# Kernel optimization log

Hardware: AMD Instinct MI355X
Metric: run time of the kernel (lower is better)

Reference implementation:

```python
import jax, jax.numpy as jnp
import numpy as np

TEMPERATURE = 0.07
BASE_TEMPERATURE = 0.07


def setup_inputs() -> dict:
    key = jax.random.key(0)
    k1, k2 = jax.random.split(key)
    features = jax.random.normal(k1, (4096, 2, 128), dtype=jnp.float32)
    labels = jax.random.randint(k2, (4096,), 0, 100, dtype=jnp.int64)
    return {"features": features, "labels": labels}


def reference(features, labels):
    # features: [B, n_views, D], labels: [B]
    B, n_views, D = features.shape
    N = B * n_views

    # label equality mask [B, B]
    lab = labels.reshape(-1, 1)
    mask = (lab == lab.T).astype(jnp.float32)

    # flatten views (C-order, same as torch .view) and L2-normalize
    feat = features.reshape(N, D)
    feat = feat / jnp.clip(jnp.linalg.norm(feat, axis=1, keepdims=True), 1e-12)

    # similarity logits [N, N]
    logits = jnp.matmul(feat, feat.T) / TEMPERATURE
    logits_max = jax.lax.stop_gradient(jnp.max(logits, axis=1, keepdims=True))
    logits = logits - logits_max

    # tile mask to [N, N] (torch .repeat ordering) and remove self-contrast
    mask = jnp.tile(mask, (n_views, n_views))
    logits_mask = 1.0 - jnp.eye(N, dtype=jnp.float32)
    mask = mask * logits_mask

    exp_logits = jnp.exp(logits) * logits_mask
    log_prob = logits - jnp.log(jnp.sum(exp_logits, axis=1, keepdims=True) + 1e-12)

    mask_pos_pairs = jnp.clip(jnp.sum(mask, axis=1), 1.0)
    mean_log_prob_pos = jnp.sum(mask * log_prob, axis=1) / mask_pos_pairs

    loss = -(TEMPERATURE / BASE_TEMPERATURE) * mean_log_prob_pos
    return jnp.mean(loss.reshape(n_views, B))
```

## Files before the change

kernel.cpp:

```cpp
#include <hip/hip_runtime.h>
#include <hip/hip_bf16.h>
#include <math.h>

#define NB 4096
#define NN 8192
#define DD 128
#define NSPLIT 16
#define CHUNK 64
#define NCHUNK 8
#define NRB 32

constexpr float INV_T = 14.285714285714286f;
constexpr float EC1   = 20.609929155556620f;
constexpr float EC0   = -20.609929155556620f;
constexpr float LN2   = 0.6931471805599453f;

typedef __attribute__((ext_vector_type(8))) short bf16x8;
typedef __attribute__((ext_vector_type(4))) float f32x4;

__device__ __forceinline__ float bf2f(ushort u) {
    union { unsigned int i; float f; } v; v.i = ((unsigned int)u) << 16; return v.f;
}

__global__ __launch_bounds__(256) void k_norm(const float* __restrict__ feat,
                                              ushort* __restrict__ fb,
                                              float* __restrict__ selfdot,
                                              float* __restrict__ out) {
    const int gid = blockIdx.x * 256 + threadIdx.x;
    if (gid == 0) out[0] = 0.0f;
    const int r    = gid >> 6;
    const int lane = threadIdx.x & 63;
    const float2 v = ((const float2*)(feat + (size_t)r * DD))[lane];
    float ss = v.x * v.x + v.y * v.y;
#pragma unroll
    for (int off = 1; off < 64; off <<= 1) ss += __shfl_xor(ss, off, 64);
    const float scale = 1.0f / fmaxf(sqrtf(ss), 1e-12f);
    __hip_bfloat162 h2;
    h2.x = __float2bfloat16(v.x * scale);
    h2.y = __float2bfloat16(v.y * scale);
    ((__hip_bfloat162*)(fb + (size_t)r * DD))[lane] = h2;
    const float xb = bf2f(((ushort2*)&h2)->x), yb = bf2f(((ushort2*)&h2)->y);
    float s2 = xb * xb + yb * yb;
#pragma unroll
    for (int off = 1; off < 64; off <<= 1) s2 += __shfl_xor(s2, off, 64);
    if (lane == 0) selfdot[r] = s2;
}

__device__ __forceinline__ void stage_chunk(const ushort* __restrict__ fb, ushort* sbuf,
                                            int jb, int w, int n15, int q) {
#pragma unroll
    for (int h = 0; h < 2; ++h) {
        const int p = w * 2 + h;
        const ushort* g = fb + (size_t)(jb + (p >> 2) * 16 + n15) * DD + (p & 3) * 32 + q * 8;
        __builtin_amdgcn_global_load_lds(
            (const __attribute__((address_space(1))) void*)g,
            (__attribute__((address_space(3))) void*)(sbuf + p * 512),
            16, 0, 0);
    }
}

__global__ __launch_bounds__(512, 2) void k_main(const ushort* __restrict__ fb,
                                                 const int* __restrict__ labels,
                                                 float* __restrict__ g_se,
                                                 float* __restrict__ g_ps,
                                                 float* __restrict__ g_ct) {
    __shared__ ushort sB[2][CHUNK * DD];
    __shared__ int slab[512];

    const int tid  = threadIdx.x;
    const int lane = tid & 63;
    const int w    = tid >> 6;
    const int rb   = blockIdx.x >> 4;
    const int js   = blockIdx.x & (NSPLIT - 1);
    const int i0   = rb * 256 + w * 32;
    const int jb0  = js * 512;
    const int q    = lane >> 4;
    const int n15  = lane & 15;

    slab[tid] = labels[(jb0 + tid) & (NB - 1)];

    bf16x8 afrag[2][4];
#pragma unroll
    for (int tt = 0; tt < 2; ++tt) {
        const ushort* rp = fb + (size_t)(i0 + tt * 16 + n15) * DD + q * 8;
#pragma unroll
        for (int kt = 0; kt < 4; ++kt) afrag[tt][kt] = *(const bf16x8*)(rp + kt * 32);
    }
    int labi[8];
#pragma unroll
    for (int tt = 0; tt < 2; ++tt)
#pragma unroll
        for (int r = 0; r < 4; ++r)
            labi[tt * 4 + r] = labels[(i0 + tt * 16 + q * 4 + r) & (NB - 1)];

    float a_se[8] = {}, a_ps[8] = {}, a_ct[8] = {};

    stage_chunk(fb, &sB[0][0], jb0, w, n15, q);
    __syncthreads();

    for (int c = 0; c < NCHUNK; ++c) {
        if (c + 1 < NCHUNK)
            stage_chunk(fb, &sB[(c + 1) & 1][0], jb0 + (c + 1) * CHUNK, w, n15, q);
        const ushort* sb = &sB[c & 1][0];
        const int crel = c * CHUNK;
#pragma unroll
        for (int jt = 0; jt < 4; ++jt) {
            bf16x8 bf[4];
#pragma unroll
            for (int kt = 0; kt < 4; ++kt)
                bf[kt] = *(const bf16x8*)(sb + (jt * 4 + kt) * 512 + lane * 8);
            const int labj = slab[crel + jt * 16 + n15];
            f32x4 a0 = {0.f, 0.f, 0.f, 0.f}, a1 = {0.f, 0.f, 0.f, 0.f};
#pragma unroll
            for (int kt = 0; kt < 4; ++kt) {
                a0 = __builtin_amdgcn_mfma_f32_16x16x32_bf16(afrag[0][kt], bf[kt], a0, 0, 0, 0);
                a1 = __builtin_amdgcn_mfma_f32_16x16x32_bf16(afrag[1][kt], bf[kt], a1, 0, 0, 0);
            }
#pragma unroll
            for (int r = 0; r < 4; ++r) {
                const float d0 = a0[r], d1 = a1[r];
                a_se[r]     += __builtin_amdgcn_exp2f(fmaf(d0, EC1, EC0));
                a_se[4 + r] += __builtin_amdgcn_exp2f(fmaf(d1, EC1, EC0));
                const bool m0 = (labi[r] == labj), m1 = (labi[4 + r] == labj);
                a_ps[r]     += m0 ? d0 : 0.0f;
                a_ps[4 + r] += m1 ? d1 : 0.0f;
                a_ct[r]     += m0 ? 1.0f : 0.0f;
                a_ct[4 + r] += m1 ? 1.0f : 0.0f;
            }
        }
        __syncthreads();
    }

#pragma unroll
    for (int s = 0; s < 8; ++s) {
        float v1 = a_se[s], v2 = a_ps[s], v3 = a_ct[s];
#pragma unroll
        for (int off = 1; off < 16; off <<= 1) {
            v1 += __shfl_xor(v1, off, 64);
            v2 += __shfl_xor(v2, off, 64);
            v3 += __shfl_xor(v3, off, 64);
        }
        if (n15 == 0) {
            const int row = i0 + (s >> 2) * 16 + q * 4 + (s & 3);
            g_se[js * NN + row] = v1;
            g_ps[js * NN + row] = v2;
            g_ct[js * NN + row] = v3;
        }
    }
}

__global__ __launch_bounds__(256) void k_final(const float* __restrict__ g_se,
                                               const float* __restrict__ g_ps,
                                               const float* __restrict__ g_ct,
                                               const float* __restrict__ selfdot,
                                               float* __restrict__ out) {
    const int r = blockIdx.x * 256 + threadIdx.x;
    float se = 0.f, ps = 0.f, ct = 0.f;
#pragma unroll
    for (int t = 0; t < NSPLIT; ++t) {
        se += g_se[t * NN + r];
        ps += g_ps[t * NN + r];
        ct += g_ct[t * NN + r];
    }
    const float sd = selfdot[r];
    se -= __builtin_amdgcn_exp2f(fmaf(sd, EC1, EC0));
    ct -= 1.0f;
    const float possum = INV_T * (ps - sd - ct);
    const float lg  = __builtin_amdgcn_logf(se + 1e-12f) * LN2;
    const float mlpp = (possum - ct * lg) / fmaxf(ct, 1.0f);
    float v = -mlpp * (1.0f / (float)NN);
#pragma unroll
    for (int off = 1; off < 64; off <<= 1) v += __shfl_xor(v, off, 64);
    __shared__ float sred[4];
    if ((threadIdx.x & 63) == 0) sred[threadIdx.x >> 6] = v;
    __syncthreads();
    if (threadIdx.x == 0) atomicAdd(out, sred[0] + sred[1] + sred[2] + sred[3]);
}

extern "C" void kernel_launch(void* const* d_in, const int* in_sizes, int n_in,
                              void* d_out, int out_size, void* d_ws, size_t ws_size,
                              hipStream_t stream) {
    const float* feat = (const float*)d_in[0];
    const int* labels = (const int*)d_in[1];
    float* out        = (float*)d_out;
    char* ws          = (char*)d_ws;

    ushort* fb      = (ushort*)ws;
    float* g_se     = (float*)(ws + (size_t)2 * 1024 * 1024);
    float* g_ps     = g_se + NSPLIT * NN;
    float* g_ct     = g_ps + NSPLIT * NN;
    float* selfdot  = g_ct + NSPLIT * NN;

    k_norm<<<NN / 4, 256, 0, stream>>>(feat, fb, selfdot, out);
    k_main<<<NRB * NSPLIT, 512, 0, stream>>>(fb, labels, g_se, g_ps, g_ct);
    k_final<<<NN / 256, 256, 0, stream>>>(g_se, g_ps, g_ct, selfdot, out);
}
```

Before: 95.30 us.

## Compute positive-pair sums via per-class feature sums and retile main kernel

Removes the label-masked positive-logit and count accumulation from the main N×N kernel. A new kernel builds per-class sums of the normalized features plus class counts. The final kernel then recovers each row's positive sum as a dot product with its class sum and derives the count from the class count. The main kernel only accumulates the exp sum and is retiled to 256-thread blocks covering 64 rows per wave, with 32 column splits. The cost is an extra launch whose LDS atomic loop runs serially over 256 rows, and a fixed class count of 100.

```diff
diff --git a/kernel.cpp b/kernel.cpp
--- a/kernel.cpp
+++ b/kernel.cpp
@@ -5,9 +5,10 @@
 #define NB 4096
 #define NN 8192
 #define DD 128
-#define NSPLIT 16
+#define NCLS 100
+#define NSPLIT 32
 #define CHUNK 64
-#define NCHUNK 8
+#define NCHUNK 4
 #define NRB 32
 
 constexpr float INV_T = 14.285714285714286f;
@@ -25,9 +26,13 @@
 __global__ __launch_bounds__(256) void k_norm(const float* __restrict__ feat,
                                               ushort* __restrict__ fb,
                                               float* __restrict__ selfdot,
+                                              float* __restrict__ zS,
+                                              int* __restrict__ counts,
                                               float* __restrict__ out) {
     const int gid = blockIdx.x * 256 + threadIdx.x;
+    if (gid < NCLS * DD + NCLS) zS[gid] = 0.0f;
     if (gid == 0) out[0] = 0.0f;
+
     const int r    = gid >> 6;
     const int lane = threadIdx.x & 63;
     const float2 v = ((const float2*)(feat + (size_t)r * DD))[lane];
@@ -46,11 +51,37 @@
     if (lane == 0) selfdot[r] = s2;
 }
 
+__global__ __launch_bounds__(256) void k_csum(const ushort* __restrict__ fb,
+                                              const int* __restrict__ labels,
+                                              float* __restrict__ S,
+                                              int* __restrict__ counts) {
+    __shared__ float Sl[NCLS * DD];
+    const int tid = threadIdx.x;
+    for (int i = tid; i < NCLS * DD; i += 256) Sl[i] = 0.0f;
+    __syncthreads();
+    const int b0   = blockIdx.x * 256;
+    const int d    = tid & 127;
+    const int half = tid >> 7;
+    int cnt_local = 0;
+    for (int i = 0; i < 256; ++i) {
+        const int b = b0 + i;
+        const int c = labels[b];
+        atomicAdd(&Sl[c * DD + d], bf2f(fb[(size_t)(b + half * NB) * DD + d]));
+        cnt_local += (tid == 0) ? 0 : 0;
+    }
+    __syncthreads();
+    for (int i = tid; i < NCLS * DD; i += 256) atomicAdd(&S[i], Sl[i]);
+    if (blockIdx.x == 0 && tid < 256) {
+        for (int b = tid * 16; b < tid * 16 + 16; ++b)
+            atomicAdd(&counts[labels[b]], 1);
+    }
+}
+
 __device__ __forceinline__ void stage_chunk(const ushort* __restrict__ fb, ushort* sbuf,
                                             int jb, int w, int n15, int q) {
 #pragma unroll
-    for (int h = 0; h < 2; ++h) {
-        const int p = w * 2 + h;
+    for (int h = 0; h < 4; ++h) {
+        const int p = w * 4 + h;
         const ushort* g = fb + (size_t)(jb + (p >> 2) * 16 + n15) * DD + (p & 3) * 32 + q * 8;
         __builtin_amdgcn_global_load_lds(
             (const __attribute__((address_space(1))) void*)g,
@@ -59,41 +90,29 @@
     }
 }
 
-__global__ __launch_bounds__(512, 2) void k_main(const ushort* __restrict__ fb,
-                                                 const int* __restrict__ labels,
-                                                 float* __restrict__ g_se,
-                                                 float* __restrict__ g_ps,
-                                                 float* __restrict__ g_ct) {
+__global__ __launch_bounds__(256, 4) void k_main(const ushort* __restrict__ fb,
+                                                 float* __restrict__ g_se) {
     __shared__ ushort sB[2][CHUNK * DD];
-    __shared__ int slab[512];
 
     const int tid  = threadIdx.x;
     const int lane = tid & 63;
     const int w    = tid >> 6;
-    const int rb   = blockIdx.x >> 4;
+    const int rb   = blockIdx.x >> 5;
     const int js   = blockIdx.x & (NSPLIT - 1);
-    const int i0   = rb * 256 + w * 32;
-    const int jb0  = js * 512;
+    const int i0   = rb * 256 + w * 64;
+    const int jb0  = js * 256;
     const int q    = lane >> 4;
     const int n15  = lane & 15;
 
-    slab[tid] = labels[(jb0 + tid) & (NB - 1)];
-
-    bf16x8 afrag[2][4];
-#pragma unroll
-    for (int tt = 0; tt < 2; ++tt) {
+    bf16x8 afrag[4][4];
+#pragma unroll
+    for (int tt = 0; tt < 4; ++tt) {
         const ushort* rp = fb + (size_t)(i0 + tt * 16 + n15) * DD + q * 8;
 #pragma unroll
         for (int kt = 0; kt < 4; ++kt) afrag[tt][kt] = *(const bf16x8*)(rp + kt * 32);
     }
-    int labi[8];
-#pragma unroll
-    for (int tt = 0; tt < 2; ++tt)
-#pragma unroll
-        for (int r = 0; r < 4; ++r)
-            labi[tt * 4 + r] = labels[(i0 + tt * 16 + q * 4 + r) & (NB - 1)];
-
-    float a_se[8] = {}, a_ps[8] = {}, a_ct[8] = {};
+
+    float a_se[16] = {};
 
     stage_chunk(fb, &sB[0][0], jb0, w, n15, q);
     __syncthreads();
@@ -102,70 +121,67 @@
         if (c + 1 < NCHUNK)
             stage_chunk(fb, &sB[(c + 1) & 1][0], jb0 + (c + 1) * CHUNK, w, n15, q);
         const ushort* sb = &sB[c & 1][0];
-        const int crel = c * CHUNK;
 #pragma unroll
         for (int jt = 0; jt < 4; ++jt) {
             bf16x8 bf[4];
 #pragma unroll
             for (int kt = 0; kt < 4; ++kt)
                 bf[kt] = *(const bf16x8*)(sb + (jt * 4 + kt) * 512 + lane * 8);
-            const int labj = slab[crel + jt * 16 + n15];
-            f32x4 a0 = {0.f, 0.f, 0.f, 0.f}, a1 = {0.f, 0.f, 0.f, 0.f};
-#pragma unroll
-            for (int kt = 0; kt < 4; ++kt) {
-                a0 = __builtin_amdgcn_mfma_f32_16x16x32_bf16(afrag[0][kt], bf[kt], a0, 0, 0, 0);
-                a1 = __builtin_amdgcn_mfma_f32_16x16x32_bf16(afrag[1][kt], bf[kt], a1, 0, 0, 0);
-            }
-#pragma unroll
-            for (int r = 0; r < 4; ++r) {
-                const float d0 = a0[r], d1 = a1[r];
-                a_se[r]     += __builtin_amdgcn_exp2f(fmaf(d0, EC1, EC0));
-                a_se[4 + r] += __builtin_amdgcn_exp2f(fmaf(d1, EC1, EC0));
-                const bool m0 = (labi[r] == labj), m1 = (labi[4 + r] == labj);
-                a_ps[r]     += m0 ? d0 : 0.0f;
-                a_ps[4 + r] += m1 ? d1 : 0.0f;
-                a_ct[r]     += m0 ? 1.0f : 0.0f;
-                a_ct[4 + r] += m1 ? 1.0f : 0.0f;
+#pragma unroll
+            for (int h = 0; h < 2; ++h) {
+                f32x4 a0 = {0.f, 0.f, 0.f, 0.f}, a1 = {0.f, 0.f, 0.f, 0.f};
+#pragma unroll
+                for (int kt = 0; kt < 4; ++kt) {
+                    a0 = __builtin_amdgcn_mfma_f32_16x16x32_bf16(afrag[2 * h][kt],     bf[kt], a0, 0, 0, 0);
+                    a1 = __builtin_amdgcn_mfma_f32_16x16x32_bf16(afrag[2 * h + 1][kt], bf[kt], a1, 0, 0, 0);
+                }
+#pragma unroll
+                for (int r = 0; r < 4; ++r) {
+                    a_se[(2 * h) * 4 + r]     += __builtin_amdgcn_exp2f(fmaf(a0[r], EC1, EC0));
+                    a_se[(2 * h + 1) * 4 + r] += __builtin_amdgcn_exp2f(fmaf(a1[r], EC1, EC0));
+                }
             }
         }
         __syncthreads();
     }
 
 #pragma unroll
-    for (int s = 0; s < 8; ++s) {
-        float v1 = a_se[s], v2 = a_ps[s], v3 = a_ct[s];
-#pragma unroll
-        for (int off = 1; off < 16; off <<= 1) {
-            v1 += __shfl_xor(v1, off, 64);
-            v2 += __shfl_xor(v2, off, 64);
-            v3 += __shfl_xor(v3, off, 64);
-        }
-        if (n15 == 0) {
-            const int row = i0 + (s >> 2) * 16 + q * 4 + (s & 3);
-            g_se[js * NN + row] = v1;
-            g_ps[js * NN + row] = v2;
-            g_ct[js * NN + row] = v3;
-        }
-    }
-}
-
-__global__ __launch_bounds__(256) void k_final(const float* __restrict__ g_se,
-                                               const float* __restrict__ g_ps,
-                                               const float* __restrict__ g_ct,
+    for (int s = 0; s < 16; ++s) {
+        float v = a_se[s];
+#pragma unroll
+        for (int off = 1; off < 16; off <<= 1) v += __shfl_xor(v, off, 64);
+        if (n15 == 0)
+            g_se[js * NN + i0 + (s >> 2) * 16 + q * 4 + (s & 3)] = v;
+    }
+}
+
+__global__ __launch_bounds__(256) void k_final(const ushort* __restrict__ fb,
+                                               const int* __restrict__ labels,
+                                               const float* __restrict__ g_se,
+                                               const float* __restrict__ S,
+                                               const int* __restrict__ counts,
                                                const float* __restrict__ selfdot,
                                                float* __restrict__ out) {
     const int r = blockIdx.x * 256 + threadIdx.x;
-    float se = 0.f, ps = 0.f, ct = 0.f;
-#pragma unroll
-    for (int t = 0; t < NSPLIT; ++t) {
-        se += g_se[t * NN + r];
-        ps += g_ps[t * NN + r];
-        ct += g_ct[t * NN + r];
+    const int c = labels[r & (NB - 1)];
+    float se = 0.0f;
+#pragma unroll
+    for (int t = 0; t < NSPLIT; ++t) se += g_se[t * NN + r];
+
+    const ushort* fp = fb + (size_t)r * DD;
+    const float*  sp = S + c * DD;
+    float s1 = 0.0f;
+#pragma unroll
+    for (int k = 0; k < DD; k += 4) {
+        ushort4 u = *(const ushort4*)(fp + k);
+        float4 sv = *(const float4*)(sp + k);
+        s1 = fmaf(bf2f(u.x), sv.x, fmaf(bf2f(u.y), sv.y,
+             fmaf(bf2f(u.z), sv.z, fmaf(bf2f(u.w), sv.w, s1))));
     }
     const float sd = selfdot[r];
     se -= __builtin_amdgcn_exp2f(fmaf(sd, EC1, EC0));
-    ct -= 1.0f;
-    const float possum = INV_T * (ps - sd - ct);
+    const float ct = (float)(2 * counts[c] - 1);
+    const float possum = INV_T * (s1 - sd - ct);
     const float lg  = __builtin_amdgcn_logf(se + 1e-12f) * LN2;
     const float mlpp = (possum - ct * lg) / fmaxf(ct, 1.0f);
     float v = -mlpp * (1.0f / (float)NN);
@@ -187,11 +203,12 @@
 
     ushort* fb      = (ushort*)ws;
     float* g_se     = (float*)(ws + (size_t)2 * 1024 * 1024);
-    float* g_ps     = g_se + NSPLIT * NN;
-    float* g_ct     = g_ps + NSPLIT * NN;
-    float* selfdot  = g_ct + NSPLIT * NN;
-
-    k_norm<<<NN / 4, 256, 0, stream>>>(feat, fb, selfdot, out);
-    k_main<<<NRB * NSPLIT, 512, 0, stream>>>(fb, labels, g_se, g_ps, g_ct);
-    k_final<<<NN / 256, 256, 0, stream>>>(g_se, g_ps, g_ct, selfdot, out);
-}
+    float* selfdot  = g_se + NSPLIT * NN;
+    float* S        = selfdot + NN;
+    int*   counts   = (int*)(S + NCLS * DD);
+
+    k_norm<<<NN / 4, 256, 0, stream>>>(feat, fb, selfdot, S, counts, out);
+    k_csum<<<NB / 256, 256, 0, stream>>>(fb, labels, S, counts);
+    k_main<<<NRB * NSPLIT, 256, 0, stream>>>(fb, g_se);
+    k_final<<<NN / 256, 256, 0, stream>>>(fb, labels, g_se, S, counts, selfdot, out);
+}
```

New measurement: 242.2 us. +154.2%, slower.

## Switch similarity GEMM to FP8 scaled MFMA and count positives via label histogram

Applied to the files above, without the earlier changes.

Normalized features are quantized to FP8 e4m3 instead of bf16, and the inner product uses the 16x16x128 f8f6f4 scaled MFMA, one instruction per tile instead of four. This halves staging bytes and LDS traffic. Positive-pair counts are no longer accumulated per element; k_final builds a per-class label histogram and derives each row's count from it, which drops one accumulator array and its global buffer. Blocks shrink to 256 threads with higher occupancy. FP8 quantization of the logits scaled by 1/0.07 risks large accuracy loss in the exp and the positive sums.

```diff
diff --git a/kernel.cpp b/kernel.cpp
--- a/kernel.cpp
+++ b/kernel.cpp
@@ -1,29 +1,28 @@
 #include <hip/hip_runtime.h>
 #include <hip/hip_bf16.h>
+#include <hip/hip_fp8.h>
 #include <math.h>
 
 #define NB 4096
 #define NN 8192
 #define DD 128
+#define NCLS 100
 #define NSPLIT 16
 #define CHUNK 64
 #define NCHUNK 8
-#define NRB 32
 
 constexpr float INV_T = 14.285714285714286f;
 constexpr float EC1   = 20.609929155556620f;
 constexpr float EC0   = -20.609929155556620f;
 constexpr float LN2   = 0.6931471805599453f;
 
-typedef __attribute__((ext_vector_type(8))) short bf16x8;
+typedef unsigned char u8;
+typedef __attribute__((ext_vector_type(8))) int   v8i;
+typedef __attribute__((ext_vector_type(4))) int   v4i;
 typedef __attribute__((ext_vector_type(4))) float f32x4;
 
-__device__ __forceinline__ float bf2f(ushort u) {
-    union { unsigned int i; float f; } v; v.i = ((unsigned int)u) << 16; return v.f;
-}
-
 __global__ __launch_bounds__(256) void k_norm(const float* __restrict__ feat,
-                                              ushort* __restrict__ fb,
+                                              u8* __restrict__ fb8,
                                               float* __restrict__ selfdot,
                                               float* __restrict__ out) {
     const int gid = blockIdx.x * 256 + threadIdx.x;
@@ -35,36 +34,35 @@
 #pragma unroll
     for (int off = 1; off < 64; off <<= 1) ss += __shfl_xor(ss, off, 64);
     const float scale = 1.0f / fmaxf(sqrtf(ss), 1e-12f);
-    __hip_bfloat162 h2;
-    h2.x = __float2bfloat16(v.x * scale);
-    h2.y = __float2bfloat16(v.y * scale);
-    ((__hip_bfloat162*)(fb + (size_t)r * DD))[lane] = h2;
-    const float xb = bf2f(((ushort2*)&h2)->x), yb = bf2f(((ushort2*)&h2)->y);
+    const __hip_fp8_e4m3 qx(v.x * scale), qy(v.y * scale);
+    const unsigned short pack = (unsigned short)qx.__x |
+                                ((unsigned short)qy.__x << 8);
+    ((unsigned short*)(fb8 + (size_t)r * DD))[lane] = pack;
+    const float xb = (float)qx, yb = (float)qy;
     float s2 = xb * xb + yb * yb;
 #pragma unroll
     for (int off = 1; off < 64; off <<= 1) s2 += __shfl_xor(s2, off, 64);
     if (lane == 0) selfdot[r] = s2;
 }
 
-__device__ __forceinline__ void stage_chunk(const ushort* __restrict__ fb, ushort* sbuf,
+__device__ __forceinline__ void stage_chunk(const u8* __restrict__ fb8, u8* sbuf,
                                             int jb, int w, int n15, int q) {
 #pragma unroll
     for (int h = 0; h < 2; ++h) {
         const int p = w * 2 + h;
-        const ushort* g = fb + (size_t)(jb + (p >> 2) * 16 + n15) * DD + (p & 3) * 32 + q * 8;
+        const u8* g = fb8 + (size_t)(jb + (p >> 1) * 16 + n15) * DD + q * 32 + (p & 1) * 16;
         __builtin_amdgcn_global_load_lds(
             (const __attribute__((address_space(1))) void*)g,
-            (__attribute__((address_space(3))) void*)(sbuf + p * 512),
+            (__attribute__((address_space(3))) void*)(sbuf + p * 1024),
             16, 0, 0);
     }
 }
 
-__global__ __launch_bounds__(512, 2) void k_main(const ushort* __restrict__ fb,
+__global__ __launch_bounds__(256, 4) void k_main(const u8* __restrict__ fb8,
                                                  const int* __restrict__ labels,
                                                  float* __restrict__ g_se,
-                                                 float* __restrict__ g_ps,
-                                                 float* __restrict__ g_ct) {
-    __shared__ ushort sB[2][CHUNK * DD];
+                                                 float* __restrict__ g_ps) {
+    __shared__ u8 sB[2][CHUNK * DD];
     __shared__ int slab[512];
 
     const int tid  = threadIdx.x;
@@ -72,19 +70,24 @@
     const int w    = tid >> 6;
     const int rb   = blockIdx.x >> 4;
     const int js   = blockIdx.x & (NSPLIT - 1);
-    const int i0   = rb * 256 + w * 32;
+    const int i0   = rb * 128 + w * 32;
     const int jb0  = js * 512;
     const int q    = lane >> 4;
     const int n15  = lane & 15;
 
-    slab[tid] = labels[(jb0 + tid) & (NB - 1)];
-
-    bf16x8 afrag[2][4];
+    slab[tid]       = labels[(jb0 + tid) & (NB - 1)];
+    slab[tid + 256] = labels[(jb0 + tid + 256) & (NB - 1)];
+
+    v8i af[2];
 #pragma unroll
     for (int tt = 0; tt < 2; ++tt) {
-        const ushort* rp = fb + (size_t)(i0 + tt * 16 + n15) * DD + q * 8;
-#pragma unroll
-        for (int kt = 0; kt < 4; ++kt) afrag[tt][kt] = *(const bf16x8*)(rp + kt * 32);
+        const u8* rp = fb8 + (size_t)(i0 + tt * 16 + n15) * DD + q * 32;
+        const v4i lo = *(const v4i*)rp;
+        const v4i hi = *(const v4i*)(rp + 16);
+        v8i a;
+#pragma unroll
+        for (int k = 0; k < 4; ++k) { a[k] = lo[k]; a[4 + k] = hi[k]; }
+        af[tt] = a;
     }
     int labi[8];
 #pragma unroll
@@ -93,39 +96,36 @@
         for (int r = 0; r < 4; ++r)
             labi[tt * 4 + r] = labels[(i0 + tt * 16 + q * 4 + r) & (NB - 1)];
 
-    float a_se[8] = {}, a_ps[8] = {}, a_ct[8] = {};
-
-    stage_chunk(fb, &sB[0][0], jb0, w, n15, q);
+    float a_se[8] = {}, a_ps[8] = {};
+
+    stage_chunk(fb8, &sB[0][0], jb0, w, n15, q);
     __syncthreads();
 
     for (int c = 0; c < NCHUNK; ++c) {
         if (c + 1 < NCHUNK)
-            stage_chunk(fb, &sB[(c + 1) & 1][0], jb0 + (c + 1) * CHUNK, w, n15, q);
-        const ushort* sb = &sB[c & 1][0];
+            stage_chunk(fb8, &sB[(c + 1) & 1][0], jb0 + (c + 1) * CHUNK, w, n15, q);
+        const u8* sb = &sB[c & 1][0];
         const int crel = c * CHUNK;
 #pragma unroll
         for (int jt = 0; jt < 4; ++jt) {
-            bf16x8 bf[4];
-#pragma unroll
-            for (int kt = 0; kt < 4; ++kt)
-                bf[kt] = *(const bf16x8*)(sb + (jt * 4 + kt) * 512 + lane * 8);
+            const v4i lo = *(const v4i*)(sb + (jt * 2 + 0) * 1024 + lane * 16);
+            const v4i hi = *(const v4i*)(sb + (jt * 2 + 1) * 1024 + lane * 16);
+            v8i bb;
+#pragma unroll
+            for (int k = 0; k < 4; ++k) { bb[k] = lo[k]; bb[4 + k] = hi[k]; }
             const int labj = slab[crel + jt * 16 + n15];
             f32x4 a0 = {0.f, 0.f, 0.f, 0.f}, a1 = {0.f, 0.f, 0.f, 0.f};
-#pragma unroll
-            for (int kt = 0; kt < 4; ++kt) {
-                a0 = __builtin_amdgcn_mfma_f32_16x16x32_bf16(afrag[0][kt], bf[kt], a0, 0, 0, 0);
-                a1 = __builtin_amdgcn_mfma_f32_16x16x32_bf16(afrag[1][kt], bf[kt], a1, 0, 0, 0);
-            }
+            a0 = __builtin_amdgcn_mfma_scale_f32_16x16x128_f8f6f4(
+                     af[0], bb, a0, 0, 0, 0, 0x7F7F7F7F, 0, 0x7F7F7F7F);
+            a1 = __builtin_amdgcn_mfma_scale_f32_16x16x128_f8f6f4(
+                     af[1], bb, a1, 0, 0, 0, 0x7F7F7F7F, 0, 0x7F7F7F7F);
 #pragma unroll
             for (int r = 0; r < 4; ++r) {
                 const float d0 = a0[r], d1 = a1[r];
                 a_se[r]     += __builtin_amdgcn_exp2f(fmaf(d0, EC1, EC0));
                 a_se[4 + r] += __builtin_amdgcn_exp2f(fmaf(d1, EC1, EC0));
-                const bool m0 = (labi[r] == labj), m1 = (labi[4 + r] == labj);
-                a_ps[r]     += m0 ? d0 : 0.0f;
-                a_ps[4 + r] += m1 ? d1 : 0.0f;
-                a_ct[r]     += m0 ? 1.0f : 0.0f;
-                a_ct[4 + r] += m1 ? 1.0f : 0.0f;
+                a_ps[r]     += (labi[r]     == labj) ? d0 : 0.0f;
+                a_ps[4 + r] += (labi[4 + r] == labj) ? d1 : 0.0f;
             }
         }
         __syncthreads();
@@ -133,48 +133,53 @@
 
 #pragma unroll
     for (int s = 0; s < 8; ++s) {
-        float v1 = a_se[s], v2 = a_ps[s], v3 = a_ct[s];
+        float v1 = a_se[s], v2 = a_ps[s];
 #pragma unroll
         for (int off = 1; off < 16; off <<= 1) {
             v1 += __shfl_xor(v1, off, 64);
             v2 += __shfl_xor(v2, off, 64);
-            v3 += __shfl_xor(v3, off, 64);
         }
         if (n15 == 0) {
             const int row = i0 + (s >> 2) * 16 + q * 4 + (s & 3);
             g_se[js * NN + row] = v1;
             g_ps[js * NN + row] = v2;
-            g_ct[js * NN + row] = v3;
         }
     }
 }
 
-__global__ __launch_bounds__(256) void k_final(const float* __restrict__ g_se,
+__global__ __launch_bounds__(256) void k_final(const int* __restrict__ labels,
+                                               const float* __restrict__ g_se,
                                                const float* __restrict__ g_ps,
-                                               const float* __restrict__ g_ct,
                                                const float* __restrict__ selfdot,
                                                float* __restrict__ out) {
-    const int r = blockIdx.x * 256 + threadIdx.x;
-    float se = 0.f, ps = 0.f, ct = 0.f;
+    __shared__ int hist[NCLS];
+    const int tid = threadIdx.x;
+    for (int i = tid; i < NCLS; i += 256) hist[i] = 0;
+    __syncthreads();
+    for (int b = tid; b < NB; b += 256) atomicAdd(&hist[labels[b]], 1);
+    __syncthreads();
+
+    const int r = blockIdx.x * 256 + tid;
+    const int c = labels[r & (NB - 1)];
+    float se = 0.f, ps = 0.f;
 #pragma unroll
     for (int t = 0; t < NSPLIT; ++t) {
         se += g_se[t * NN + r];
         ps += g_ps[t * NN + r];
-        ct += g_ct[t * NN + r];
     }
     const float sd = selfdot[r];
     se -= __builtin_amdgcn_exp2f(fmaf(sd, EC1, EC0));
-    ct -= 1.0f;
-    const float possum = INV_T * (ps - sd - ct);
+    const float ct = (float)(2 * hist[c] - 1);
+    const float possum = INV_T * ((ps - sd) - ct);
     const float lg  = __builtin_amdgcn_logf(se + 1e-12f) * LN2;
     const float mlpp = (possum - ct * lg) / fmaxf(ct, 1.0f);
     float v = -mlpp * (1.0f / (float)NN);
 #pragma unroll
     for (int off = 1; off < 64; off <<= 1) v += __shfl_xor(v, off, 64);
     __shared__ float sred[4];
-    if ((threadIdx.x & 63) == 0) sred[threadIdx.x >> 6] = v;
-    __syncthreads();
-    if (threadIdx.x == 0) atomicAdd(out, sred[0] + sred[1] + sred[2] + sred[3]);
+    if ((tid & 63) == 0) sred[tid >> 6] = v;
+    __syncthreads();
+    if (tid == 0) atomicAdd(out, sred[0] + sred[1] + sred[2] + sred[3]);
 }
 
 extern "C" void kernel_launch(void* const* d_in, const int* in_sizes, int n_in,
@@ -185,13 +190,12 @@
     float* out        = (float*)d_out;
     char* ws          = (char*)d_ws;
 
-    ushort* fb      = (ushort*)ws;
-    float* g_se     = (float*)(ws + (size_t)2 * 1024 * 1024);
+    u8* fb8         = (u8*)ws;
+    float* g_se     = (float*)(ws + (size_t)1 * 1024 * 1024);
     float* g_ps     = g_se + NSPLIT * NN;
-    float* g_ct     = g_ps + NSPLIT * NN;
-    float* selfdot  = g_ct + NSPLIT * NN;
-
-    k_norm<<<NN / 4, 256, 0, stream>>>(feat, fb, selfdot, out);
-    k_main<<<NRB * NSPLIT, 512, 0, stream>>>(fb, labels, g_se, g_ps, g_ct);
-    k_final<<<NN / 256, 256, 0, stream>>>(g_se, g_ps, g_ct, selfdot, out);
-}
+    float* selfdot  = g_ps + NSPLIT * NN;
+
+    k_norm<<<NN / 4, 256, 0, stream>>>(feat, fb8, selfdot, out);
+    k_main<<<(NN / 128) * NSPLIT, 256, 0, stream>>>(fb8, labels, g_se, g_ps);
+    k_final<<<NN / 256, 256, 0, stream>>>(labels, g_se, g_ps, selfdot, out);
+}
```

Result: faster. 82.97 us (-12.9%).
